# Optimization experiments

Measured on AMD Instinct MI355X. Metric: run time of the kernel, lower is better.

The kernel has to match this reference:

```python
import jax, jax.numpy as jnp
import numpy as np

B, IN_CH, HID, H, W = 8, 64, 128, 128, 128
WS, NHEADS = 4, 4
HD = HID // NHEADS
GROUPS = 8  # min(8, hidden_ch)
EPS = 1e-5


def setup_inputs() -> dict:
    key = jax.random.key(0)
    ks = jax.random.split(key, 8)
    def w(k, shape):
        return jax.random.normal(k, shape, jnp.float32) * 0.02
    return {
        "x": jax.random.normal(ks[0], (B, IN_CH, H, W), jnp.float32),
        "h": jax.random.normal(ks[1], (B, HID, H, W), jnp.float32),
        "c": jax.random.normal(ks[2], (B, HID, H, W), jnp.float32),
        "Wproj": w(ks[3], (HID, IN_CH + HID)),
        "bproj": jnp.zeros((HID,), jnp.float32),
        "ln_g": jnp.ones((HID,), jnp.float32),
        "ln_b": jnp.zeros((HID,), jnp.float32),
        "Wqkv": w(ks[4], (3 * HID, HID)),
        "bqkv": jnp.zeros((3 * HID,), jnp.float32),
        "Wo": w(ks[5], (HID, HID)),
        "bo": jnp.zeros((HID,), jnp.float32),
        "Wgates": w(ks[6], (4 * HID, HID)),
        "bgates": jnp.zeros((4 * HID,), jnp.float32),
        "gn_g": jnp.ones((HID,), jnp.float32),
        "gn_b": jnp.zeros((HID,), jnp.float32),
    }


def group_norm(x, g, b):
    # x: [B, C, H, W], normalize per (group, spatial)
    Bx, C, Hx, Wx = x.shape
    xg = x.reshape(Bx, GROUPS, C // GROUPS, Hx, Wx)
    mu = xg.mean(axis=(2, 3, 4), keepdims=True)
    var = xg.var(axis=(2, 3, 4), keepdims=True)
    xn = ((xg - mu) * jax.lax.rsqrt(var + EPS)).reshape(Bx, C, Hx, Wx)
    return xn * g[:, None, None] + b[:, None, None]


def reference(x, h, c, Wproj, bproj, ln_g, ln_b, Wqkv, bqkv, Wo, bo,
              Wgates, bgates, gn_g, gn_b):
    # 1x1 conv input projection on concat(x, h)
    comb = jnp.concatenate([x, h], axis=1)  # [B, in+hid, H, W]
    proj = jnp.einsum('bihw,oi->bohw', comb, Wproj) + bproj[:, None, None]

    # window partition (H, W divisible by WS -> no padding)
    nh, nw = H // WS, W // WS
    xw = proj.reshape(B, HID, nh, WS, nw, WS)
    xw = xw.transpose(0, 2, 4, 3, 5, 1).reshape(B * nh * nw, WS * WS, HID)

    # LocalWindowAttention: LayerNorm -> QKV -> MHSA -> proj
    mu = xw.mean(axis=-1, keepdims=True)
    var = xw.var(axis=-1, keepdims=True)
    xn = (xw - mu) * jax.lax.rsqrt(var + EPS) * ln_g + ln_b
    qkv = (xn @ Wqkv.T + bqkv).reshape(-1, WS * WS, 3, NHEADS, HD)
    q = qkv[:, :, 0].transpose(0, 2, 1, 3)  # [Bw, nh, N, hd]
    k = qkv[:, :, 1].transpose(0, 2, 1, 3)
    v = qkv[:, :, 2].transpose(0, 2, 1, 3)
    scale = HD ** -0.5
    attn = jax.nn.softmax(jnp.einsum('whnd,whmd->whnm', q, k) * scale, axis=-1)
    out = jnp.einsum('whnm,whmd->whnd', attn, v)
    out = out.transpose(0, 2, 1, 3).reshape(-1, WS * WS, HID)
    out = out @ Wo.T + bo

    # window unpartition -> [B, C, H, W]
    attn_map = out.reshape(B, nh, nw, WS, WS, HID)
    attn_map = attn_map.transpose(0, 5, 1, 3, 2, 4).reshape(B, HID, H, W)
    attn_map = group_norm(attn_map, gn_g, gn_b)

    # conv-gated LSTM update (1x1 conv gates)
    gates = jnp.einsum('bchw,oc->bohw', attn_map, Wgates) + bgates[:, None, None]
    ci, cf, co, cg = jnp.split(gates, 4, axis=1)
    i = jax.nn.sigmoid(ci)
    f = jax.nn.sigmoid(cf)
    o = jax.nn.sigmoid(co)
    g = jnp.tanh(cg)
    cnext = f * c + i * g
    hnext = group_norm(o * jnp.tanh(cnext), gn_g, gn_b)
    return hnext, cnext
```

## Files before the change

### kernel.cpp

```cpp
#include <hip/hip_runtime.h>
#include <math.h>

typedef unsigned int uint;
typedef unsigned short ushort;
typedef short s16x8 __attribute__((ext_vector_type(8)));
typedef float f32x4 __attribute__((ext_vector_type(4)));

#define PIX 16384
#define EPSF 1e-5f

__device__ __forceinline__ ushort f2bf(float f) {
  union { float f; uint u; } v; v.f = f;
  uint u = v.u;
  uint r = (u + 0x7FFFu + ((u >> 16) & 1u)) >> 16;
  return (ushort)r;
}
__device__ __forceinline__ float bf2f(ushort h) {
  union { uint u; float f; } v; v.u = ((uint)h) << 16;
  return v.f;
}
__device__ __forceinline__ uint pk2(float a, float b) {
  return (uint)f2bf(a) | ((uint)f2bf(b) << 16);
}
__device__ __forceinline__ float fsigmoid(float v) { return 1.f / (1.f + __expf(-v)); }
__device__ __forceinline__ float ftanh(float v) { return 1.f - 2.f / (__expf(2.f * v) + 1.f); }

union Frag { uint4 u4; uint u[4]; s16x8 s; };

__global__ void k_prep(const float* __restrict__ Wp, const float* __restrict__ Wq,
                       const float* __restrict__ Wo, const float* __restrict__ Wg,
                       const float* __restrict__ ln_g,
                       ushort* __restrict__ FWp, ushort* __restrict__ FWq,
                       ushort* __restrict__ FWo, ushort* __restrict__ FWg) {
  int idx = blockIdx.x * 256 + threadIdx.x;
  const float* W; ushort* F; int KS, ldw, rel; bool scale = false;
  if (idx < 3072)       { W = Wp; F = FWp; KS = 6; ldw = 192; rel = idx; }
  else if (idx < 9216)  { W = Wq; F = FWq; KS = 4; ldw = 128; rel = idx - 3072; scale = true; }
  else if (idx < 11264) { W = Wo; F = FWo; KS = 4; ldw = 128; rel = idx - 9216; }
  else                  { W = Wg; F = FWg; KS = 4; ldw = 128; rel = idx - 11264; }
  int l = rel & 63, rest = rel >> 6;
  int ks = rest % KS, mt = rest / KS;
  int col = ks * 32 + (l >> 4) * 8;
  const float* src = W + (size_t)(mt * 16 + (l & 15)) * ldw + col;
  float g[8] = {1.f, 1.f, 1.f, 1.f, 1.f, 1.f, 1.f, 1.f};
  if (scale) {
    #pragma unroll
    for (int j = 0; j < 8; j++) g[j] = ln_g[col + j];
  }
  uint4 v;
  v.x = pk2(src[0] * g[0], src[1] * g[1]);
  v.y = pk2(src[2] * g[2], src[3] * g[3]);
  v.z = pk2(src[4] * g[4], src[5] * g[5]);
  v.w = pk2(src[6] * g[6], src[7] * g[7]);
  *reinterpret_cast<uint4*>(F + (size_t)rel * 8) = v;
}

__global__ void k_prep2(const float* __restrict__ Wq, const float* __restrict__ ln_g,
                        const float* __restrict__ ln_b, const float* __restrict__ bqkv,
                        float* __restrict__ Sarr, float* __restrict__ Tbarr) {
  int o = threadIdx.x;
  if (o >= 384) return;
  float S = 0.f, T = 0.f;
  const float* wr = Wq + (size_t)o * 128;
  for (int i = 0; i < 128; i++) {
    float wv = wr[i];
    S = fmaf(wv, ln_g[i], S);
    T = fmaf(wv, ln_b[i], T);
  }
  Sarr[o] = S;
  Tbarr[o] = T + bqkv[o];
}

__global__ __launch_bounds__(256, 2) void k_attn(
    const float* __restrict__ x, const float* __restrict__ h,
    const ushort* __restrict__ FWp, const float* __restrict__ bproj,
    const ushort* __restrict__ FWq, const float* __restrict__ Sarr,
    const float* __restrict__ Tbarr,
    const ushort* __restrict__ FWoT, const float* __restrict__ bo,
    ushort* __restrict__ attn_map, float* __restrict__ stA_raw)
{
  __shared__ __align__(16) char LM[67584];
  __shared__ float sSum[64], sSum2[64];
  __shared__ float sStat[16];

  const int t = threadIdx.x;
  const int bid = blockIdx.x;
  const int b = bid >> 8, wh = (bid >> 3) & 31, ww0 = bid & 7;
  const int w = t >> 6, l = t & 63, q = l >> 4, r16 = l & 15;

  uint* sInP = (uint*)LM;
  ushort* sXn = (ushort*)LM;

  if (t < 64) { sSum[t] = 0.f; sSum2[t] = 0.f; }
  if (t < 16) sStat[t] = 0.f;

  {
    const float* xb = x + (size_t)b * 64 * PIX;
    const float* hb = h + (size_t)b * 128 * PIX;
    #pragma unroll
    for (int it = 0; it < 6; it++) {
      int item = it * 256 + t;
      int wv = item & 3, r = (item >> 2) & 3, chp = item >> 4;
      int ch0 = chp * 2;
      int gpix = (wh * 4 + r) * 128 + ww0 * 16 + wv * 4;
      float4 a, c2;
      if (ch0 < 64) {
        a  = *reinterpret_cast<const float4*>(xb + (size_t)ch0 * PIX + gpix);
        c2 = *reinterpret_cast<const float4*>(xb + (size_t)(ch0 + 1) * PIX + gpix);
      } else {
        a  = *reinterpret_cast<const float4*>(hb + (size_t)(ch0 - 64) * PIX + gpix);
        c2 = *reinterpret_cast<const float4*>(hb + (size_t)(ch0 - 63) * PIX + gpix);
      }
      uint4 pkd;
      pkd.x = pk2(a.x, c2.x); pkd.y = pk2(a.y, c2.y);
      pkd.z = pk2(a.z, c2.z); pkd.w = pk2(a.w, c2.w);
      *reinterpret_cast<uint4*>(sInP + chp * 68 + wv * 16 + r * 4) = pkd;
    }
  }
  __syncthreads();

  f32x4 acc1[2][4];
  {
    #pragma unroll
    for (int mi = 0; mi < 2; mi++)
      #pragma unroll
      for (int nt = 0; nt < 4; nt++) acc1[mi][nt] = (f32x4){0.f, 0.f, 0.f, 0.f};
    for (int ks = 0; ks < 6; ks++) {
      Frag bf[4];
      #pragma unroll
      for (int nt = 0; nt < 4; nt++)
        #pragma unroll
        for (int s = 0; s < 4; s++)
          bf[nt].u[s] = sInP[(ks * 16 + q * 4 + s) * 68 + nt * 16 + r16];
      #pragma unroll
      for (int mi = 0; mi < 2; mi++) {
        Frag af;
        af.u4 = *reinterpret_cast<const uint4*>(FWp + (((w + mi * 4) * 6 + ks) * 64 + l) * 8);
        #pragma unroll
        for (int nt = 0; nt < 4; nt++)
          acc1[mi][nt] = __builtin_amdgcn_mfma_f32_16x16x32_bf16(af.s, bf[nt].s, acc1[mi][nt], 0, 0, 0);
      }
    }
  }
  __syncthreads();

  {
    float pst[4] = {0.f, 0.f, 0.f, 0.f}, pst2[4] = {0.f, 0.f, 0.f, 0.f};
    #pragma unroll
    for (int mi = 0; mi < 2; mi++) {
      int o0 = (w + mi * 4) * 16 + q * 4;
      const float4 bv = *reinterpret_cast<const float4*>(bproj + o0);
      #pragma unroll
      for (int nt = 0; nt < 4; nt++) {
        float v0 = acc1[mi][nt][0] + bv.x, v1 = acc1[mi][nt][1] + bv.y;
        float v2 = acc1[mi][nt][2] + bv.z, v3 = acc1[mi][nt][3] + bv.w;
        uint2 pk; pk.x = pk2(v0, v1); pk.y = pk2(v2, v3);
        *reinterpret_cast<uint2*>(sXn + (nt * 16 + r16) * 136 + o0) = pk;
        pst[nt]  += v0 + v1 + v2 + v3;
        pst2[nt] += v0 * v0 + v1 * v1 + v2 * v2 + v3 * v3;
      }
    }
    #pragma unroll
    for (int nt = 0; nt < 4; nt++) {
      float s = pst[nt], s2 = pst2[nt];
      s  += __shfl_xor(s, 16);  s  += __shfl_xor(s, 32);
      s2 += __shfl_xor(s2, 16); s2 += __shfl_xor(s2, 32);
      if (q == 0) {
        atomicAdd(&sSum[nt * 16 + r16], s);
        atomicAdd(&sSum2[nt * 16 + r16], s2);
      }
    }
  }
  __syncthreads();

  {
    f32x4 acc2[6][4];
    #pragma unroll
    for (int mi = 0; mi < 6; mi++)
      #pragma unroll
      for (int nt = 0; nt < 4; nt++) acc2[mi][nt] = (f32x4){0.f, 0.f, 0.f, 0.f};
    for (int ks = 0; ks < 4; ks++) {
      Frag bf[4];
      #pragma unroll
      for (int nt = 0; nt < 4; nt++)
        bf[nt].u4 = *reinterpret_cast<const uint4*>(sXn + (nt * 16 + r16) * 136 + ks * 32 + q * 8);
      #pragma unroll
      for (int mi = 0; mi < 6; mi++) {
        Frag af;
        af.u4 = *reinterpret_cast<const uint4*>(FWq + (((w + mi * 4) * 4 + ks) * 64 + l) * 8);
        #pragma unroll
        for (int nt = 0; nt < 4; nt++)
          acc2[mi][nt] = __builtin_amdgcn_mfma_f32_16x16x32_bf16(af.s, bf[nt].s, acc2[mi][nt], 0, 0, 0);
      }
    }
    float rstd_[4], mr_[4];
    #pragma unroll
    for (int nt = 0; nt < 4; nt++) {
      int tok = nt * 16 + r16;
      float mu = sSum[tok] * 0.0078125f;
      float var = sSum2[tok] * 0.0078125f - mu * mu;
      rstd_[nt] = rsqrtf(var + EPSF);
      mr_[nt] = -mu * rstd_[nt];
    }
    ushort* sQKu = (ushort*)(LM + 17408);
    ushort* sVu  = (ushort*)(LM + 51200);
    #pragma unroll
    for (int mi = 0; mi < 6; mi++) {
      int mt = w + mi * 4;
      int oo = mt * 16 + q * 4;
      const float4 S4  = *reinterpret_cast<const float4*>(Sarr + oo);
      const float4 Tb4 = *reinterpret_cast<const float4*>(Tbarr + oo);
      #pragma unroll
      for (int nt = 0; nt < 4; nt++) {
        float v0 = fmaf(rstd_[nt], acc2[mi][nt][0], fmaf(mr_[nt], S4.x, Tb4.x));
        float v1 = fmaf(rstd_[nt], acc2[mi][nt][1], fmaf(mr_[nt], S4.y, Tb4.y));
        float v2 = fmaf(rstd_[nt], acc2[mi][nt][2], fmaf(mr_[nt], S4.z, Tb4.z));
        float v3 = fmaf(rstd_[nt], acc2[mi][nt][3], fmaf(mr_[nt], S4.w, Tb4.w));
        if (mi < 4) {
          uint2 pk; pk.x = pk2(v0, v1); pk.y = pk2(v2, v3);
          *reinterpret_cast<uint2*>(sQKu + nt * 4224 + r16 * 264 + oo) = pk;
        } else {
          ushort* vd = sVu + nt * 2048 + (oo - 256) * 16 + r16;
          vd[0] = f2bf(v0); vd[16] = f2bf(v1); vd[32] = f2bf(v2); vd[48] = f2bf(v3);
        }
      }
    }
  }
  __syncthreads();

  {
    const float scale = 0.17677669529663687f;
    ushort* sQKw = (ushort*)(LM + 17408 + w * 8448);
    ushort* sPw  = (ushort*)(LM + w * 4096);
    Frag af4[4], bf4[4];
    #pragma unroll
    for (int hd = 0; hd < 4; hd++) {
      af4[hd].u4 = *reinterpret_cast<const uint4*>(sQKw + r16 * 264 + hd * 32 + q * 8);
      bf4[hd].u4 = *reinterpret_cast<const uint4*>(sQKw + r16 * 264 + 128 + hd * 32 + q * 8);
    }
    #pragma unroll
    for (int hd = 0; hd < 4; hd++) {
      if (l < 32) {
        int row = l >> 1, hz = l & 1;
        uint4 z = {0u, 0u, 0u, 0u};
        *reinterpret_cast<uint4*>(sPw + hd * 512 + row * 32 + 16 + hz * 8) = z;
      }
    }
    f32x4 sc[4];
    #pragma unroll
    for (int hd = 0; hd < 4; hd++) {
      f32x4 z4 = (f32x4){0.f, 0.f, 0.f, 0.f};
      sc[hd] = __builtin_amdgcn_mfma_f32_16x16x32_bf16(af4[hd].s, bf4[hd].s, z4, 0, 0, 0);
    }
    #pragma unroll
    for (int hd = 0; hd < 4; hd++) {
      ushort* pd = sPw + hd * 512 + (q * 4) * 32 + r16;
      #pragma unroll
      for (int r = 0; r < 4; r++) {
        float sv = sc[hd][r] * scale;
        float mx = sv;
        mx = fmaxf(mx, __shfl_xor(mx, 1));
        mx = fmaxf(mx, __shfl_xor(mx, 2));
        mx = fmaxf(mx, __shfl_xor(mx, 4));
        mx = fmaxf(mx, __shfl_xor(mx, 8));
        float e = __expf(sv - mx);
        float sm = e;
        sm += __shfl_xor(sm, 1); sm += __shfl_xor(sm, 2);
        sm += __shfl_xor(sm, 4); sm += __shfl_xor(sm, 8);
        pd[r * 32] = f2bf(e / sm);
      }
    }
    ushort* sOw = (ushort*)(LM + 17408 + w * 8448 + 4096);
    ushort* sVw = (ushort*)(LM + 51200) + w * 2048;
    #pragma unroll
    for (int hd = 0; hd < 4; hd++) {
      Frag pa;
      pa.u4 = *reinterpret_cast<const uint4*>(sPw + hd * 512 + r16 * 32 + q * 8);
      #pragma unroll
      for (int nt2 = 0; nt2 < 2; nt2++) {
        int ch = hd * 32 + nt2 * 16 + r16;
        int off = (q < 2) ? q * 8 : 0;
        Frag vf;
        vf.u4 = *reinterpret_cast<const uint4*>(sVw + ch * 16 + off);
        f32x4 z4 = (f32x4){0.f, 0.f, 0.f, 0.f};
        f32x4 o4 = __builtin_amdgcn_mfma_f32_16x16x32_bf16(pa.s, vf.s, z4, 0, 0, 0);
        ushort* od = sOw + (q * 4) * 136 + ch;
        od[0] = f2bf(o4[0]); od[136] = f2bf(o4[1]);
        od[272] = f2bf(o4[2]); od[408] = f2bf(o4[3]);
      }
    }
  }
  __syncthreads();

  {
    ushort* sFinu = (ushort*)(LM + 51200);
    Frag a4[4][4];
    #pragma unroll
    for (int nt = 0; nt < 4; nt++) {
      ushort* sOnt = (ushort*)(LM + 17408 + nt * 8448 + 4096);
      #pragma unroll
      for (int ks = 0; ks < 4; ks++)
        a4[nt][ks].u4 = *reinterpret_cast<const uint4*>(sOnt + r16 * 136 + ks * 32 + q * 8);
    }
    #pragma unroll
    for (int mi2 = 0; mi2 < 2; mi2++) {
      int ntg = w + mi2 * 4;
      f32x4 acw[4];
      #pragma unroll
      for (int nt = 0; nt < 4; nt++) acw[nt] = (f32x4){0.f, 0.f, 0.f, 0.f};
      #pragma unroll
      for (int ks = 0; ks < 4; ks++) {
        Frag bfw;
        bfw.u4 = *reinterpret_cast<const uint4*>(FWoT + ((ntg * 4 + ks) * 64 + l) * 8);
        #pragma unroll
        for (int nt = 0; nt < 4; nt++)
          acw[nt] = __builtin_amdgcn_mfma_f32_16x16x32_bf16(a4[nt][ks].s, bfw.s, acw[nt], 0, 0, 0);
      }
      int ch = ntg * 16 + r16;
      float bb = bo[ch];
      #pragma unroll
      for (int nt = 0; nt < 4; nt++) {
        uint2 pk;
        pk.x = pk2(acw[nt][0] + bb, acw[nt][1] + bb);
        pk.y = pk2(acw[nt][2] + bb, acw[nt][3] + bb);
        *reinterpret_cast<uint2*>(sFinu + nt * 2048 + ch * 16 + q * 4) = pk;
      }
    }
  }
  __syncthreads();

  {
    ushort* sFinu = (ushort*)(LM + 51200);
    #pragma unroll
    for (int it = 0; it < 4; it++) {
      int seg = it * 256 + t;
      int ch = seg >> 3, r = (seg >> 1) & 3, half = seg & 1;
      const ushort* f0 = sFinu + (half * 2    ) * 2048;
      const ushort* f1 = sFinu + (half * 2 + 1) * 2048;
      uint2 a  = *reinterpret_cast<const uint2*>(f0 + ch * 16 + r * 4);
      uint2 c2 = *reinterpret_cast<const uint2*>(f1 + ch * 16 + r * 4);
      uint4 val = {a.x, a.y, c2.x, c2.y};
      *reinterpret_cast<uint4*>(attn_map + (size_t)(b * 128 + ch) * PIX
                                + (wh * 4 + r) * 128 + ww0 * 16 + half * 8) = val;
      float sv = 0.f, sv2 = 0.f;
      uint uu[4] = {val.x, val.y, val.z, val.w};
      #pragma unroll
      for (int k2 = 0; k2 < 4; k2++) {
        float fv0 = bf2f((ushort)(uu[k2] & 0xFFFFu));
        float fv1 = bf2f((ushort)(uu[k2] >> 16));
        sv += fv0 + fv1; sv2 += fv0 * fv0 + fv1 * fv1;
      }
      sv  += __shfl_xor(sv, 1);  sv  += __shfl_xor(sv, 2);  sv  += __shfl_xor(sv, 4);
      sv2 += __shfl_xor(sv2, 1); sv2 += __shfl_xor(sv2, 2); sv2 += __shfl_xor(sv2, 4);
      if ((t & 7) == 0) {
        int g = ch >> 4;
        atomicAdd(&sStat[g * 2], sv);
        atomicAdd(&sStat[g * 2 + 1], sv2);
      }
    }
  }
  __syncthreads();
  if (t < 16) atomicAdd(&stA_raw[b * 16 + t], sStat[t]);
}

__global__ __launch_bounds__(256, 4) void k_gates(
    const ushort* __restrict__ attn_map, const float* __restrict__ stA_raw,
    const float* __restrict__ gn_g, const float* __restrict__ gn_b,
    const ushort* __restrict__ FWg, const float* __restrict__ bgates,
    const float* __restrict__ c, float* __restrict__ cnext,
    ushort* __restrict__ tbuf, float* __restrict__ stB_raw)
{
  __shared__ uint sG2[32 * 66];
  __shared__ float sA[128], sB[128];
  __shared__ float sStat[16];
  const int t = threadIdx.x, bid = blockIdx.x;
  const int b = bid >> 9, p0 = (bid & 511) * 32;
  const int w = t >> 6, l = t & 63, q = l >> 4, r16 = l & 15;

  if (t < 128) {
    int g = t >> 4;
    const float invN = 1.f / 262144.f;
    float mu = stA_raw[b * 16 + g * 2] * invN;
    float var = stA_raw[b * 16 + g * 2 + 1] * invN - mu * mu;
    float rs = rsqrtf(var + EPSF);
    float A = rs * gn_g[t];
    sA[t] = A; sB[t] = gn_b[t] - mu * A;
  }
  if (t >= 240) sStat[t - 240] = 0.f;
  __syncthreads();

  {
    int pr = t >> 2, px0 = (t & 3) * 8;
    int c0 = pr * 2;
    const ushort* ab = attn_map + (size_t)(b * 128) * PIX + p0 + px0;
    uint4 a0 = *reinterpret_cast<const uint4*>(ab + (size_t)c0 * PIX);
    uint4 a1 = *reinterpret_cast<const uint4*>(ab + (size_t)(c0 + 1) * PIX);
    float A0 = sA[c0], B0 = sB[c0], A1 = sA[c0 + 1], B1 = sB[c0 + 1];
    uint u0[4] = {a0.x, a0.y, a0.z, a0.w};
    uint u1[4] = {a1.x, a1.y, a1.z, a1.w};
    #pragma unroll
    for (int j = 0; j < 4; j++) {
      float v0lo = bf2f((ushort)(u0[j] & 0xFFFFu)) * A0 + B0;
      float v0hi = bf2f((ushort)(u0[j] >> 16)) * A0 + B0;
      float v1lo = bf2f((ushort)(u1[j] & 0xFFFFu)) * A1 + B1;
      float v1hi = bf2f((ushort)(u1[j] >> 16)) * A1 + B1;
      sG2[(px0 + 2 * j) * 66 + pr]     = pk2(v0lo, v1lo);
      sG2[(px0 + 2 * j + 1) * 66 + pr] = pk2(v0hi, v1hi);
    }
  }

  float4 cv[2][2];
  #pragma unroll
  for (int j = 0; j < 2; j++) {
    int ch = (w + 4 * j) * 16 + r16;
    const float* cb = c + (size_t)(b * 128 + ch) * PIX + p0 + q * 4;
    cv[j][0] = *reinterpret_cast<const float4*>(cb);
    cv[j][1] = *reinterpret_cast<const float4*>(cb + 16);
  }
  __syncthreads();

  f32x4 acc[4][2][2];
  #pragma unroll
  for (int g2 = 0; g2 < 4; g2++)
    #pragma unroll
    for (int j = 0; j < 2; j++)
      #pragma unroll
      for (int pxt = 0; pxt < 2; pxt++) acc[g2][j][pxt] = (f32x4){0.f, 0.f, 0.f, 0.f};

  const ushort* sGu = (const ushort*)sG2;
  for (int ks = 0; ks < 4; ks++) {
    Frag af[2];
    #pragma unroll
    for (int pxt = 0; pxt < 2; pxt++)
      af[pxt].u4 = *reinterpret_cast<const uint4*>(sGu + (pxt * 16 + r16) * 132 + ks * 32 + q * 8);
    #pragma unroll
    for (int g2 = 0; g2 < 4; g2++) {
      #pragma unroll
      for (int j = 0; j < 2; j++) {
        int ct = w + 4 * j + 8 * g2;
        Frag bfw;
        bfw.u4 = *reinterpret_cast<const uint4*>(FWg + ((ct * 4 + ks) * 64 + l) * 8);
        #pragma unroll
        for (int pxt = 0; pxt < 2; pxt++)
          acc[g2][j][pxt] = __builtin_amdgcn_mfma_f32_16x16x32_bf16(af[pxt].s, bfw.s, acc[g2][j][pxt], 0, 0, 0);
      }
    }
  }

  float gs[2] = {0.f, 0.f}, gs2[2] = {0.f, 0.f};
  #pragma unroll
  for (int j = 0; j < 2; j++) {
    int ch = (w + 4 * j) * 16 + r16;
    float bi = bgates[ch], bff = bgates[128 + ch], bog = bgates[256 + ch], bgg = bgates[384 + ch];
    #pragma unroll
    for (int pxt = 0; pxt < 2; pxt++) {
      size_t gbase = (size_t)(b * 128 + ch) * PIX + p0 + pxt * 16 + q * 4;
      const float cc[4] = {cv[j][pxt].x, cv[j][pxt].y, cv[j][pxt].z, cv[j][pxt].w};
      float cn[4], tv[4];
      #pragma unroll
      for (int r = 0; r < 4; r++) {
        float ig = fsigmoid(acc[0][j][pxt][r] + bi);
        float fg = fsigmoid(acc[1][j][pxt][r] + bff);
        float og = fsigmoid(acc[2][j][pxt][r] + bog);
        float gg = ftanh   (acc[3][j][pxt][r] + bgg);
        cn[r] = fg * cc[r] + ig * gg;
        tv[r] = og * ftanh(cn[r]);
        gs[j] += tv[r]; gs2[j] += tv[r] * tv[r];
      }
      float4 cno = {cn[0], cn[1], cn[2], cn[3]};
      *reinterpret_cast<float4*>(cnext + gbase) = cno;
      uint2 tpk;
      tpk.x = pk2(tv[0], tv[1]); tpk.y = pk2(tv[2], tv[3]);
      *reinterpret_cast<uint2*>(tbuf + gbase) = tpk;
    }
  }
  #pragma unroll
  for (int j = 0; j < 2; j++) {
    float s = gs[j], s2 = gs2[j];
    s += __shfl_xor(s, 1); s += __shfl_xor(s, 2); s += __shfl_xor(s, 4);
    s += __shfl_xor(s, 8); s += __shfl_xor(s, 16); s += __shfl_xor(s, 32);
    s2 += __shfl_xor(s2, 1); s2 += __shfl_xor(s2, 2); s2 += __shfl_xor(s2, 4);
    s2 += __shfl_xor(s2, 8); s2 += __shfl_xor(s2, 16); s2 += __shfl_xor(s2, 32);
    if (l == 0) {
      int g = w + 4 * j;
      atomicAdd(&sStat[g * 2], s);
      atomicAdd(&sStat[g * 2 + 1], s2);
    }
  }
  __syncthreads();
  if (t < 16) atomicAdd(&stB_raw[b * 16 + t], sStat[t]);
}

__global__ __launch_bounds__(256) void k_gnout(
    const ushort* __restrict__ tbuf, const float* __restrict__ stB_raw,
    const float* __restrict__ gn_g, const float* __restrict__ gn_b,
    float* __restrict__ hnext)
{
  size_t idx = ((size_t)blockIdx.x * 256 + threadIdx.x) * 8;
  if (idx >= (size_t)16777216) return;
  int chrow = (int)(idx >> 14);
  int b = chrow >> 7, ch = chrow & 127, g = ch >> 4;
  const float invN = 1.f / 262144.f;
  float mu = stB_raw[b * 16 + g * 2] * invN;
  float var = stB_raw[b * 16 + g * 2 + 1] * invN - mu * mu;
  float rstd = rsqrtf(var + EPSF);
  float A = gn_g[ch] * rstd, Bv = gn_b[ch] - mu * A;
  uint4 u = *reinterpret_cast<const uint4*>(tbuf + idx);
  float4 o0, o1;
  o0.x = bf2f((ushort)(u.x & 0xFFFFu)) * A + Bv;
  o0.y = bf2f((ushort)(u.x >> 16)) * A + Bv;
  o0.z = bf2f((ushort)(u.y & 0xFFFFu)) * A + Bv;
  o0.w = bf2f((ushort)(u.y >> 16)) * A + Bv;
  o1.x = bf2f((ushort)(u.z & 0xFFFFu)) * A + Bv;
  o1.y = bf2f((ushort)(u.z >> 16)) * A + Bv;
  o1.z = bf2f((ushort)(u.w & 0xFFFFu)) * A + Bv;
  o1.w = bf2f((ushort)(u.w >> 16)) * A + Bv;
  *reinterpret_cast<float4*>(hnext + idx) = o0;
  *reinterpret_cast<float4*>(hnext + idx + 4) = o1;
}

extern "C" void kernel_launch(void* const* d_in, const int* in_sizes, int n_in,
                              void* d_out, int out_size, void* d_ws, size_t ws_size,
                              hipStream_t stream) {
  (void)in_sizes; (void)n_in; (void)out_size; (void)ws_size;
  const float* x      = (const float*)d_in[0];
  const float* h      = (const float*)d_in[1];
  const float* c      = (const float*)d_in[2];
  const float* Wproj  = (const float*)d_in[3];
  const float* bproj  = (const float*)d_in[4];
  const float* ln_g   = (const float*)d_in[5];
  const float* ln_b   = (const float*)d_in[6];
  const float* Wqkv   = (const float*)d_in[7];
  const float* bqkv   = (const float*)d_in[8];
  const float* Wo     = (const float*)d_in[9];
  const float* bo     = (const float*)d_in[10];
  const float* Wgates = (const float*)d_in[11];
  const float* bgates = (const float*)d_in[12];
  const float* gn_g   = (const float*)d_in[13];
  const float* gn_b   = (const float*)d_in[14];

  float* out = (float*)d_out;
  float* hnext = out;
  float* cnext = out + 16777216;

  char* W = (char*)d_ws;
  ushort* attn = (ushort*)W;
  ushort* tbuf = (ushort*)(W + 33554432);
  size_t off = 67108864;
  ushort* FWp = (ushort*)(W + off); off += 49152;
  ushort* FWq = (ushort*)(W + off); off += 98304;
  ushort* FWo = (ushort*)(W + off); off += 32768;
  ushort* FWg = (ushort*)(W + off); off += 131072;
  float* stA_raw = (float*)(W + off); off += 512;
  float* stB_raw = (float*)(W + off); off += 512;
  float* Sarr    = (float*)(W + off); off += 1536;
  float* Tbarr   = (float*)(W + off); off += 1536;

  hipMemsetAsync(stA_raw, 0, 1024, stream);

  k_prep<<<76, 256, 0, stream>>>(Wproj, Wqkv, Wo, Wgates, ln_g, FWp, FWq, FWo, FWg);
  k_prep2<<<1, 384, 0, stream>>>(Wqkv, ln_g, ln_b, bqkv, Sarr, Tbarr);

  k_attn<<<2048, 256, 0, stream>>>(x, h, FWp, bproj, FWq, Sarr, Tbarr,
                                   FWo, bo, attn, stA_raw);
  k_gates<<<4096, 256, 0, stream>>>(attn, stA_raw, gn_g, gn_b, FWg, bgates,
                                    c, cnext, tbuf, stB_raw);
  k_gnout<<<8192, 256, 0, stream>>>(tbuf, stB_raw, gn_g, gn_b, hnext);
}
```

Baseline: 225.7 us.

## Shrink attention LDS footprint via buffer aliasing to fit three blocks per CU

Result: faster. 215.3 us (-4.6%).

```diff
diff --git a/kernel.cpp b/kernel.cpp
--- a/kernel.cpp
+++ b/kernel.cpp
@@ -71,7 +71,7 @@
   Tbarr[o] = T + bqkv[o];
 }
 
-__global__ __launch_bounds__(256, 2) void k_attn(
+__global__ __launch_bounds__(256, 3) void k_attn(
     const float* __restrict__ x, const float* __restrict__ h,
     const ushort* __restrict__ FWp, const float* __restrict__ bproj,
     const ushort* __restrict__ FWq, const float* __restrict__ Sarr,
@@ -79,7 +79,7 @@
     const ushort* __restrict__ FWoT, const float* __restrict__ bo,
     ushort* __restrict__ attn_map, float* __restrict__ stA_raw)
 {
-  __shared__ __align__(16) char LM[67584];
+  __shared__ __align__(16) char LM[51200];
   __shared__ float sSum[64], sSum2[64];
   __shared__ float sStat[16];
 
@@ -173,27 +173,16 @@
   }
   __syncthreads();
 
-  {
-    f32x4 acc2[6][4];
-    #pragma unroll
-    for (int mi = 0; mi < 6; mi++)
-      #pragma unroll
-      for (int nt = 0; nt < 4; nt++) acc2[mi][nt] = (f32x4){0.f, 0.f, 0.f, 0.f};
-    for (int ks = 0; ks < 4; ks++) {
-      Frag bf[4];
+  float rstd_[4], mr_[4];
+  f32x4 accV[2][4];
+  {
+    Frag bfh[4][4];
+    #pragma unroll
+    for (int ks = 0; ks < 4; ks++)
       #pragma unroll
       for (int nt = 0; nt < 4; nt++)
-        bf[nt].u4 = *reinterpret_cast<const uint4*>(sXn + (nt * 16 + r16) * 136 + ks * 32 + q * 8);
-      #pragma unroll
-      for (int mi = 0; mi < 6; mi++) {
-        Frag af;
-        af.u4 = *reinterpret_cast<const uint4*>(FWq + (((w + mi * 4) * 4 + ks) * 64 + l) * 8);
-        #pragma unroll
-        for (int nt = 0; nt < 4; nt++)
-          acc2[mi][nt] = __builtin_amdgcn_mfma_f32_16x16x32_bf16(af.s, bf[nt].s, acc2[mi][nt], 0, 0, 0);
-      }
-    }
-    float rstd_[4], mr_[4];
+        bfh[ks][nt].u4 = *reinterpret_cast<const uint4*>(sXn + (nt * 16 + r16) * 136 + ks * 32 + q * 8);
+
     #pragma unroll
     for (int nt = 0; nt < 4; nt++) {
       int tok = nt * 16 + r16;
@@ -202,27 +191,68 @@
       rstd_[nt] = rsqrtf(var + EPSF);
       mr_[nt] = -mu * rstd_[nt];
     }
+
     ushort* sQKu = (ushort*)(LM + 17408);
-    ushort* sVu  = (ushort*)(LM + 51200);
-    #pragma unroll
-    for (int mi = 0; mi < 6; mi++) {
+    #pragma unroll
+    for (int mi = 0; mi < 4; mi++) {
       int mt = w + mi * 4;
+      f32x4 accq[4];
+      #pragma unroll
+      for (int nt = 0; nt < 4; nt++) accq[nt] = (f32x4){0.f, 0.f, 0.f, 0.f};
+      #pragma unroll
+      for (int ks = 0; ks < 4; ks++) {
+        Frag af;
+        af.u4 = *reinterpret_cast<const uint4*>(FWq + ((mt * 4 + ks) * 64 + l) * 8);
+        #pragma unroll
+        for (int nt = 0; nt < 4; nt++)
+          accq[nt] = __builtin_amdgcn_mfma_f32_16x16x32_bf16(af.s, bfh[ks][nt].s, accq[nt], 0, 0, 0);
+      }
       int oo = mt * 16 + q * 4;
       const float4 S4  = *reinterpret_cast<const float4*>(Sarr + oo);
       const float4 Tb4 = *reinterpret_cast<const float4*>(Tbarr + oo);
       #pragma unroll
       for (int nt = 0; nt < 4; nt++) {
-        float v0 = fmaf(rstd_[nt], acc2[mi][nt][0], fmaf(mr_[nt], S4.x, Tb4.x));
-        float v1 = fmaf(rstd_[nt], acc2[mi][nt][1], fmaf(mr_[nt], S4.y, Tb4.y));
-        float v2 = fmaf(rstd_[nt], acc2[mi][nt][2], fmaf(mr_[nt], S4.z, Tb4.z));
-        float v3 = fmaf(rstd_[nt], acc2[mi][nt][3], fmaf(mr_[nt], S4.w, Tb4.w));
-        if (mi < 4) {
-          uint2 pk; pk.x = pk2(v0, v1); pk.y = pk2(v2, v3);
-          *reinterpret_cast<uint2*>(sQKu + nt * 4224 + r16 * 264 + oo) = pk;
-        } else {
-          ushort* vd = sVu + nt * 2048 + (oo - 256) * 16 + r16;
-          vd[0] = f2bf(v0); vd[16] = f2bf(v1); vd[32] = f2bf(v2); vd[48] = f2bf(v3);
-        }
+        float v0 = fmaf(rstd_[nt], accq[nt][0], fmaf(mr_[nt], S4.x, Tb4.x));
+        float v1 = fmaf(rstd_[nt], accq[nt][1], fmaf(mr_[nt], S4.y, Tb4.y));
+        float v2 = fmaf(rstd_[nt], accq[nt][2], fmaf(mr_[nt], S4.z, Tb4.z));
+        float v3 = fmaf(rstd_[nt], accq[nt][3], fmaf(mr_[nt], S4.w, Tb4.w));
+        uint2 pk; pk.x = pk2(v0, v1); pk.y = pk2(v2, v3);
+        *reinterpret_cast<uint2*>(sQKu + nt * 4224 + r16 * 264 + oo) = pk;
+      }
+    }
+    #pragma unroll
+    for (int mi = 0; mi < 2; mi++) {
+      int mt = w + 16 + mi * 4;
+      #pragma unroll
+      for (int nt = 0; nt < 4; nt++) accV[mi][nt] = (f32x4){0.f, 0.f, 0.f, 0.f};
+      #pragma unroll
+      for (int ks = 0; ks < 4; ks++) {
+        Frag af;
+        af.u4 = *reinterpret_cast<const uint4*>(FWq + ((mt * 4 + ks) * 64 + l) * 8);
+        #pragma unroll
+        for (int nt = 0; nt < 4; nt++)
+          accV[mi][nt] = __builtin_amdgcn_mfma_f32_16x16x32_bf16(af.s, bfh[ks][nt].s, accV[mi][nt], 0, 0, 0);
+      }
+    }
+  }
+  __syncthreads();
+
+  {
+    ushort* sVu = (ushort*)LM;
+    #pragma unroll
+    for (int mi = 0; mi < 2; mi++) {
+      int mt = w + 16 + mi * 4;
+      int oo = mt * 16 + q * 4;
+      const float4 S4  = *reinterpret_cast<const float4*>(Sarr + oo);
+      const float4 Tb4 = *reinterpret_cast<const float4*>(Tbarr + oo);
+      #pragma unroll
+      for (int nt = 0; nt < 4; nt++) {
+        float v0 = fmaf(rstd_[nt], accV[mi][nt][0], fmaf(mr_[nt], S4.x, Tb4.x));
+        float v1 = fmaf(rstd_[nt], accV[mi][nt][1], fmaf(mr_[nt], S4.y, Tb4.y));
+        float v2 = fmaf(rstd_[nt], accV[mi][nt][2], fmaf(mr_[nt], S4.z, Tb4.z));
+        float v3 = fmaf(rstd_[nt], accV[mi][nt][3], fmaf(mr_[nt], S4.w, Tb4.w));
+        ushort* vd = sVu + nt * 2048 + (oo - 256) * 16 + r16;
+        vd[0] = f2bf(v0); vd[16] = f2bf(v1); vd[32] = f2bf(v2); vd[48] = f2bf(v3);
       }
     }
   }
@@ -231,7 +261,7 @@
   {
     const float scale = 0.17677669529663687f;
     ushort* sQKw = (ushort*)(LM + 17408 + w * 8448);
-    ushort* sPw  = (ushort*)(LM + w * 4096);
+    ushort* sPw  = sQKw;
     Frag af4[4], bf4[4];
     #pragma unroll
     for (int hd = 0; hd < 4; hd++) {
@@ -270,8 +300,8 @@
         pd[r * 32] = f2bf(e / sm);
       }
     }
-    ushort* sOw = (ushort*)(LM + 17408 + w * 8448 + 4096);
-    ushort* sVw = (ushort*)(LM + 51200) + w * 2048;
+    ushort* sOw = sQKw + 2048;
+    ushort* sVw = (ushort*)LM + w * 2048;
     #pragma unroll
     for (int hd = 0; hd < 4; hd++) {
       Frag pa;
@@ -293,7 +323,7 @@
   __syncthreads();
 
   {
-    ushort* sFinu = (ushort*)(LM + 51200);
+    ushort* sFinu = (ushort*)LM;
     Frag a4[4][4];
     #pragma unroll
     for (int nt = 0; nt < 4; nt++) {
@@ -330,7 +360,7 @@
   __syncthreads();
 
   {
-    ushort* sFinu = (ushort*)(LM + 51200);
+    ushort* sFinu = (ushort*)LM;
     #pragma unroll
     for (int it = 0; it < 4; it++) {
       int seg = it * 256 + t;
```
